# Performance work log

Hardware: AMD Instinct MI355X
Metric: run time of the kernel (lower is better)

The kernel has to match this reference:

```python
import jax, jax.numpy as jnp
import numpy as np

B, S, D, H, HD = 2, 2048, 1024, 16, 64
SCALE = HD ** -0.5


def setup_inputs() -> dict:
    key = jax.random.key(0)
    ks = jax.random.split(key, 11)
    w = 0.02
    return {
        "query": jax.random.normal(ks[0], (B, S, D), jnp.float32),
        "key": jax.random.normal(ks[1], (B, S, D), jnp.float32),
        "value": jax.random.normal(ks[2], (B, S, D), jnp.float32),
        "Wq": jax.random.normal(ks[3], (D, H * HD), jnp.float32) * w,
        "bq": jnp.zeros((H * HD,), jnp.float32),
        "Wk": jax.random.normal(ks[4], (D, H * HD), jnp.float32) * w,
        "bk": jnp.zeros((H * HD,), jnp.float32),
        "Wv": jax.random.normal(ks[5], (D, H * HD), jnp.float32) * w,
        "bv": jnp.zeros((H * HD,), jnp.float32),
        "Wo": jax.random.normal(ks[6], (H * HD, D), jnp.float32) * w,
        "bo": jnp.zeros((D,), jnp.float32),
    }


def reference(query, key, value, Wq, bq, Wk, bk, Wv, bv, Wo, bo):
    # projections -> [B, H, S, HD]
    q = (query @ Wq + bq).reshape(B, S, H, HD).transpose(0, 2, 1, 3)
    k = (key @ Wk + bk).reshape(B, S, H, HD).transpose(0, 2, 1, 3)
    v = (value @ Wv + bv).reshape(B, S, H, HD).transpose(0, 2, 1, 3)
    # attention scores [B, H, S, S]
    attn_score = jnp.einsum("bhqd,bhkd->bhqk", q, k) * SCALE
    attn_weights = jax.nn.softmax(attn_score, axis=-1)
    out = jnp.einsum("bhqk,bhkd->bhqd", attn_weights, v)
    out = out.transpose(0, 2, 1, 3).reshape(B, S, H * HD)
    out = out @ Wo + bo
    return out, attn_weights
```

## Files before the change

### kernel.cpp

```cpp
#include <hip/hip_runtime.h>
#include <hip/hip_bf16.h>
#include <stdint.h>

#define B_ 2
#define S_ 2048
#define D_ 1024
#define H_ 16
#define HD_ 64
#define SCALE_ 0.125f
#define SC2_ 0.18033688011112042f

typedef __attribute__((ext_vector_type(8))) short bfx8;
typedef __attribute__((ext_vector_type(4))) float f32x4;

#define VWAIT(n) asm volatile("s_waitcnt vmcnt(" #n ")" ::: "memory")

__device__ __forceinline__ void gld_lds16(const void* g, void* l) {
    __builtin_amdgcn_global_load_lds(
        (const __attribute__((address_space(1))) void*)g,
        (__attribute__((address_space(3))) void*)l, 16, 0, 0);
}

__global__ __launch_bounds__(256) void prep(
    const float* __restrict__ a, const float* __restrict__ b, const float* __restrict__ c,
    __hip_bfloat16* __restrict__ oa, __hip_bfloat16* __restrict__ ob, __hip_bfloat16* __restrict__ oc,
    const float* __restrict__ w0, const float* __restrict__ w1,
    const float* __restrict__ w2, const float* __restrict__ w3,
    __hip_bfloat16* __restrict__ o0, __hip_bfloat16* __restrict__ o1,
    __hip_bfloat16* __restrict__ o2, __hip_bfloat16* __restrict__ o3)
{
    __shared__ float t[32][33];
    const int bid = blockIdx.x;
    if (bid < 12288) {
        const int which = bid >> 12;
        const int xb = bid & 4095;
        const float* src = which == 0 ? a : which == 1 ? b : c;
        __hip_bfloat16* dst = which == 0 ? oa : which == 1 ? ob : oc;
        const size_t i = ((size_t)xb * 256 + threadIdx.x) * 4;
        float4 v = *(const float4*)(src + i);
        ushort4 u;
        __hip_bfloat16 tt;
        tt = __float2bfloat16(v.x); u.x = *(unsigned short*)&tt;
        tt = __float2bfloat16(v.y); u.y = *(unsigned short*)&tt;
        tt = __float2bfloat16(v.z); u.z = *(unsigned short*)&tt;
        tt = __float2bfloat16(v.w); u.w = *(unsigned short*)&tt;
        *(ushort4*)(dst + i) = u;
    } else {
        const int tb = bid - 12288;
        const int z = tb >> 10;
        const int rem = tb & 1023;
        const int bx = (rem & 31) * 32, by = (rem >> 5) * 32;
        const float* W = z == 0 ? w0 : z == 1 ? w1 : z == 2 ? w2 : w3;
        __hip_bfloat16* Wt = z == 0 ? o0 : z == 1 ? o1 : z == 2 ? o2 : o3;
        const int x = threadIdx.x & 31, y = threadIdx.x >> 5;
#pragma unroll
        for (int i = 0; i < 32; i += 8)
            t[y + i][x] = W[(size_t)(by + y + i) * 1024 + bx + x];
        __syncthreads();
#pragma unroll
        for (int i = 0; i < 32; i += 8)
            Wt[(size_t)(bx + y + i) * 1024 + by + x] = __float2bfloat16(t[x][y + i]);
    }
}

__global__ __launch_bounds__(256) void transpose_v(
    const __hip_bfloat16* __restrict__ vn,
    __hip_bfloat16* __restrict__ vtb)
{
    __shared__ unsigned int t[64][65];
    const int bh = blockIdx.y;
    const int st = blockIdx.x;
    const int tid = threadIdx.x, lane = tid & 63, w = tid >> 6;
    {
        const int sl = tid >> 2, c0 = (tid & 3) * 16;
        const ushort4* src = (const ushort4*)(vn + ((size_t)bh * S_ + st * 64 + sl) * 64 + c0);
        ushort4 a = src[0], b = src[1], c = src[2], d = src[3];
        unsigned short vals[16] = {a.x,a.y,a.z,a.w,b.x,b.y,b.z,b.w,
                                   c.x,c.y,c.z,c.w,d.x,d.y,d.z,d.w};
#pragma unroll
        for (int j = 0; j < 16; ++j) t[sl][c0 + j] = vals[j];
    }
    __syncthreads();
    const int sl2 = (lane & 31) * 2;
    const int dh  = (lane >> 5) * 8;
#pragma unroll
    for (int j = 0; j < 8; ++j) {
        const int d = w * 16 + dh + j;
        const unsigned int lo = t[sl2][d], hi = t[sl2 + 1][d];
        const unsigned int pk = (lo & 0xFFFFu) | (hi << 16);
        *(unsigned int*)(vtb + ((size_t)bh * HD_ + d) * S_ + st * 64 + sl2) = pk;
    }
}

__device__ __forceinline__ void gemm_body(
    const __hip_bfloat16* __restrict__ A,
    const __hip_bfloat16* __restrict__ Bt,
    const float* __restrict__ bias,
    void* __restrict__ Cout, int mode,
    __hip_bfloat16 (*As)[128 * 32], __hip_bfloat16 (*Bs)[128 * 32],
    int bm, int bn)
{
    constexpr int K = 1024, N = 1024;
    const int tid = threadIdx.x;
    const int wid = tid >> 6, lane = tid & 63;
    const int wm = (wid >> 1) * 64, wn = (wid & 1) * 64;

    f32x4 acc[4][4] = {};

    const int srow = lane >> 2;
    const int scol = (lane & 3) * 8;

    auto stage = [&](int kt, int buf) {
#pragma unroll
        for (int i = 0; i < 2; ++i) {
            const int rb = wid * 32 + i * 16;
            gld_lds16(A  + (size_t)(bm + rb + srow) * K + kt * 32 + scol, (char*)As[buf] + rb * 64);
            gld_lds16(Bt + (size_t)(bn + rb + srow) * K + kt * 32 + scol, (char*)Bs[buf] + rb * 64);
        }
    };

    stage(0, 0);
    __syncthreads();

    for (int kt = 0; kt < K / 32; ++kt) {
        const int cur = kt & 1;
        if (kt < K / 32 - 1) stage(kt + 1, cur ^ 1);
        bfx8 af[4], bf[4];
#pragma unroll
        for (int m = 0; m < 4; ++m)
            af[m] = *(const bfx8*)((const char*)As[cur] + (wm + m * 16 + (lane & 15)) * 64 + (lane >> 4) * 16);
#pragma unroll
        for (int n = 0; n < 4; ++n)
            bf[n] = *(const bfx8*)((const char*)Bs[cur] + (wn + n * 16 + (lane & 15)) * 64 + (lane >> 4) * 16);
        __builtin_amdgcn_s_setprio(1);
#pragma unroll
        for (int m = 0; m < 4; ++m)
#pragma unroll
            for (int n = 0; n < 4; ++n)
                acc[m][n] = __builtin_amdgcn_mfma_f32_16x16x32_bf16(af[m], bf[n], acc[m][n], 0, 0, 0);
        __builtin_amdgcn_s_setprio(0);
        __syncthreads();
    }

#pragma unroll
    for (int m = 0; m < 4; ++m) {
        const int row0 = bm + wm + m * 16 + ((lane >> 4) << 2);
#pragma unroll
        for (int n = 0; n < 4; ++n) {
            const int col = bn + wn + n * 16 + (lane & 15);
            const float bv = bias[col];
#pragma unroll
            for (int r = 0; r < 4; ++r) {
                const int i = row0 + r;
                const float v = acc[m][n][r] + bv;
                if (mode == 2) {
                    ((float*)Cout)[(size_t)i * N + col] = v;
                } else {
                    const int b = i >> 11, s = i & 2047, h = col >> 6, d = col & 63;
                    ((__hip_bfloat16*)Cout)[(((size_t)b * H_ + h) * S_ + s) * HD_ + d] = __float2bfloat16(v);
                }
            }
        }
    }
}

__global__ __launch_bounds__(256, 3) void gemm_qkv(
    const __hip_bfloat16* __restrict__ xq, const __hip_bfloat16* __restrict__ xk,
    const __hip_bfloat16* __restrict__ xv,
    const __hip_bfloat16* __restrict__ Wqt, const __hip_bfloat16* __restrict__ Wkt,
    const __hip_bfloat16* __restrict__ Wvt,
    const float* __restrict__ bq, const float* __restrict__ bk, const float* __restrict__ bv,
    __hip_bfloat16* __restrict__ qb, __hip_bfloat16* __restrict__ kbuf,
    __hip_bfloat16* __restrict__ vnb)
{
    __shared__ __align__(16) __hip_bfloat16 As[2][128 * 32];
    __shared__ __align__(16) __hip_bfloat16 Bs[2][128 * 32];
    const int z = blockIdx.z;
    const __hip_bfloat16* A  = z == 0 ? xq : z == 1 ? xk : xv;
    const __hip_bfloat16* Bt = z == 0 ? Wqt : z == 1 ? Wkt : Wvt;
    const float* bias        = z == 0 ? bq : z == 1 ? bk : bv;
    void* out                = z == 0 ? (void*)qb : z == 1 ? (void*)kbuf : (void*)vnb;
    gemm_body(A, Bt, bias, out, 0, As, Bs, blockIdx.x * 128, blockIdx.y * 128);
}

__global__ __launch_bounds__(256, 2) void gemm_wo(
    const __hip_bfloat16* __restrict__ A, const __hip_bfloat16* __restrict__ Bt,
    const float* __restrict__ bias, float* __restrict__ Cout)
{
    constexpr int K = 1024, N = 1024;
    __shared__ __align__(16) __hip_bfloat16 As[2][128 * 32];
    __shared__ __align__(16) __hip_bfloat16 Bs[2][64 * 32];
    const int tid = threadIdx.x;
    const int wid = tid >> 6, lane = tid & 63;
    const int wm = (wid >> 1) * 64, wn = (wid & 1) * 32;
    const int bm = blockIdx.x * 128, bn = blockIdx.y * 64;

    f32x4 acc[4][2] = {};

    const int srow = lane >> 2;
    const int scol = (lane & 3) * 8;

    auto stage = [&](int kt, int buf) {
#pragma unroll
        for (int i = 0; i < 2; ++i) {
            const int rb = wid * 32 + i * 16;
            gld_lds16(A + (size_t)(bm + rb + srow) * K + kt * 32 + scol, (char*)As[buf] + rb * 64);
        }
        const int rbB = wid * 16;
        gld_lds16(Bt + (size_t)(bn + rbB + srow) * K + kt * 32 + scol, (char*)Bs[buf] + rbB * 64);
    };

    stage(0, 0);
    __syncthreads();

    for (int kt = 0; kt < K / 32; ++kt) {
        const int cur = kt & 1;
        if (kt < K / 32 - 1) stage(kt + 1, cur ^ 1);
        bfx8 af[4], bf[2];
#pragma unroll
        for (int m = 0; m < 4; ++m)
            af[m] = *(const bfx8*)((const char*)As[cur] + (wm + m * 16 + (lane & 15)) * 64 + (lane >> 4) * 16);
#pragma unroll
        for (int n = 0; n < 2; ++n)
            bf[n] = *(const bfx8*)((const char*)Bs[cur] + (wn + n * 16 + (lane & 15)) * 64 + (lane >> 4) * 16);
        __builtin_amdgcn_s_setprio(1);
#pragma unroll
        for (int m = 0; m < 4; ++m)
#pragma unroll
            for (int n = 0; n < 2; ++n)
                acc[m][n] = __builtin_amdgcn_mfma_f32_16x16x32_bf16(af[m], bf[n], acc[m][n], 0, 0, 0);
        __builtin_amdgcn_s_setprio(0);
        __syncthreads();
    }

#pragma unroll
    for (int m = 0; m < 4; ++m) {
        const int row0 = bm + wm + m * 16 + ((lane >> 4) << 2);
#pragma unroll
        for (int n = 0; n < 2; ++n) {
            const int col = bn + wn + n * 16 + (lane & 15);
            const float bv = bias[col];
#pragma unroll
            for (int r = 0; r < 4; ++r)
                Cout[(size_t)(row0 + r) * N + col] = acc[m][n][r] + bv;
        }
    }
}

__global__ __launch_bounds__(256, 4) void attn_fused(
    const __hip_bfloat16* __restrict__ qb,
    const __hip_bfloat16* __restrict__ kb,
    const __hip_bfloat16* __restrict__ vt,
    float* __restrict__ attnw,
    __hip_bfloat16* __restrict__ aout)
{
    __shared__ __align__(16) char lds_[40960];
    char* const ps_ = lds_ + 32768;

    const int wg  = blockIdx.x;
    const int lin = (wg & 7) * 128 + (wg >> 3);
    const int bh  = lin >> 5;
    const int qt  = lin & 31;

    const int tid = threadIdx.x, wid = tid >> 6, lane = tid & 63;
    const int qrow0 = qt * 64 + wid * 16;

    const char* kh = (const char*)(kb + (size_t)bh * S_ * HD_);
    const char* vh = (const char*)(vt + (size_t)bh * HD_ * S_);

    bfx8 qf[2];
#pragma unroll
    for (int kx = 0; kx < 2; ++kx)
        qf[kx] = *(const bfx8*)(qb + ((size_t)bh * S_ + qrow0 + (lane & 15)) * HD_
                                 + kx * 32 + (lane >> 4) * 8);

    const int sr = lane >> 3;
    const int sc = lane & 7;

    auto stage_k = [&](int kt, char* dst) {
#pragma unroll
        for (int i = 0; i < 2; ++i) {
            const int rb = wid * 16 + i * 8;
            const int row = rb + sr;
            const int colb = (sc * 16) ^ ((row & 7) << 4);
            gld_lds16(kh + (size_t)(kt * 64 + row) * 128 + colb, dst + rb * 128);
        }
    };
    auto stage_v = [&](int kt, char* dst) {
#pragma unroll
        for (int i = 0; i < 2; ++i) {
            const int rb = wid * 16 + i * 8;
            const int row = rb + sr;
            const int colb = (sc * 16) ^ ((row & 7) << 4);
            gld_lds16(vh + ((size_t)row * S_ + kt * 64) * 2 + colb, dst + rb * 128);
        }
    };

    float lsum = 0.f;
    stage_k(0, lds_);
    stage_k(1, lds_ + 8192);
    for (int kt = 0; kt < 32; ++kt) {
        if (kt < 30) {
            stage_k(kt + 2, lds_ + ((kt + 2) & 3) * 8192);
            VWAIT(4);
        } else if (kt == 30) { VWAIT(2); } else { VWAIT(0); }
        __builtin_amdgcn_sched_barrier(0);
        __builtin_amdgcn_s_barrier();

        const char* kbase = lds_ + (kt & 3) * 8192;
        f32x4 c[4] = {};
#pragma unroll
        for (int kx = 0; kx < 2; ++kx) {
            bfx8 bfv[4];
#pragma unroll
            for (int cf = 0; cf < 4; ++cf) {
                const int row = cf * 16 + (lane & 15);
                bfv[cf] = *(const bfx8*)(kbase + row * 128
                                          + ((kx * 64 + (lane >> 4) * 16) ^ ((row & 7) << 4)));
            }
            __builtin_amdgcn_s_setprio(1);
#pragma unroll
            for (int cf = 0; cf < 4; ++cf)
                c[cf] = __builtin_amdgcn_mfma_f32_16x16x32_bf16(bfv[cf], qf[kx], c[cf], 0, 0, 0);
            __builtin_amdgcn_s_setprio(0);
        }
#pragma unroll
        for (int cf = 0; cf < 4; ++cf)
            lsum += exp2f(c[cf][0] * SC2_) + exp2f(c[cf][1] * SC2_)
                  + exp2f(c[cf][2] * SC2_) + exp2f(c[cf][3] * SC2_);
    }
    float llog;
    {
        float s = lsum;
        s += __shfl_xor(s, 16);
        s += __shfl_xor(s, 32);
        llog = -__log2f(s);
    }

    f32x4 o[4] = {};
    stage_k(0, lds_);
    stage_v(0, lds_ + 16384);
    VWAIT(0);
    __builtin_amdgcn_s_barrier();
    for (int kt = 0; kt < 32; ++kt) {
        const int cur = kt & 1;
        const char* ksb = lds_ + cur * 8192;
        const char* vsb = lds_ + 16384 + cur * 8192;

        if (kt < 31) {
            stage_k(kt + 1, lds_ + (cur ^ 1) * 8192);
            stage_v(kt + 1, lds_ + 16384 + (cur ^ 1) * 8192);
        }

        f32x4 c[4] = {};
#pragma unroll
        for (int kx = 0; kx < 2; ++kx) {
            bfx8 bfv[4];
#pragma unroll
            for (int cf = 0; cf < 4; ++cf) {
                const int row = cf * 16 + (lane & 15);
                bfv[cf] = *(const bfx8*)(ksb + row * 128
                                          + ((kx * 64 + (lane >> 4) * 16) ^ ((row & 7) << 4)));
            }
            __builtin_amdgcn_s_setprio(1);
#pragma unroll
            for (int cf = 0; cf < 4; ++cf)
                c[cf] = __builtin_amdgcn_mfma_f32_16x16x32_bf16(bfv[cf], qf[kx], c[cf], 0, 0, 0);
            __builtin_amdgcn_s_setprio(0);
        }

        {
            const int q = lane & 15;
            char* const prow_base = ps_ + (wid * 16 + q) * 128;
            const int swz = (q & 7) << 4;
#pragma unroll
            for (int cf = 0; cf < 4; ++cf) {
                const int k0b = (cf * 16 + (lane >> 4) * 4) * 2;
                ushort4 pk;
                __hip_bfloat16 bb;
                bb = __float2bfloat16(exp2f(fmaf(c[cf][0], SC2_, llog))); pk.x = *(unsigned short*)&bb;
                bb = __float2bfloat16(exp2f(fmaf(c[cf][1], SC2_, llog))); pk.y = *(unsigned short*)&bb;
                bb = __float2bfloat16(exp2f(fmaf(c[cf][2], SC2_, llog))); pk.z = *(unsigned short*)&bb;
                bb = __float2bfloat16(exp2f(fmaf(c[cf][3], SC2_, llog))); pk.w = *(unsigned short*)&bb;
                *(ushort4*)(prow_base + (k0b ^ swz)) = pk;
            }
        }

#pragma unroll
        for (int rr = 0; rr < 4; ++rr) {
            const int p = wid * 16 + rr * 4 + (lane >> 4);
            const uint2 u = *(const uint2*)(ps_ + p * 128
                                            + (((lane & 15) * 8) ^ ((p & 7) << 4)));
            f32x4 f;
            f[0] = __uint_as_float(u.x << 16);
            f[1] = __uint_as_float(u.x & 0xFFFF0000u);
            f[2] = __uint_as_float(u.y << 16);
            f[3] = __uint_as_float(u.y & 0xFFFF0000u);
            __builtin_nontemporal_store(f,
                (f32x4*)(attnw + ((size_t)bh * S_ + qt * 64 + p) * S_ + kt * 64 + (lane & 15) * 4));
        }

#pragma unroll
        for (int kx = 0; kx < 2; ++kx) {
            bfx8 pf, vf[4];
            {
                const int prow = wid * 16 + (lane & 15);
                pf = *(const bfx8*)(ps_ + prow * 128
                                     + ((kx * 64 + (lane >> 4) * 16) ^ ((prow & 7) << 4)));
            }
#pragma unroll
            for (int df = 0; df < 4; ++df) {
                const int vrow = df * 16 + (lane & 15);
                vf[df] = *(const bfx8*)(vsb + vrow * 128
                                         + ((kx * 64 + (lane >> 4) * 16) ^ ((vrow & 7) << 4)));
            }
            __builtin_amdgcn_s_setprio(1);
#pragma unroll
            for (int df = 0; df < 4; ++df)
                o[df] = __builtin_amdgcn_mfma_f32_16x16x32_bf16(pf, vf[df], o[df], 0, 0, 0);
            __builtin_amdgcn_s_setprio(0);
        }

        if (kt < 31) {
            VWAIT(4);
            __builtin_amdgcn_sched_barrier(0);
            __builtin_amdgcn_s_barrier();
        }
    }

    const int b = bh >> 4, h = bh & 15;
#pragma unroll
    for (int r = 0; r < 4; ++r) {
        const int s = qrow0 + ((lane >> 4) << 2) + r;
#pragma unroll
        for (int df = 0; df < 4; ++df) {
            const int d = df * 16 + (lane & 15);
            aout[((size_t)b * S_ + s) * D_ + h * HD_ + d] = __float2bfloat16(o[df][r]);
        }
    }
}

extern "C" void kernel_launch(void* const* d_in, const int* in_sizes, int n_in,
                              void* d_out, int out_size, void* d_ws, size_t ws_size,
                              hipStream_t stream)
{
    (void)in_sizes; (void)n_in; (void)out_size; (void)ws_size;
    const float* query = (const float*)d_in[0];
    const float* key_  = (const float*)d_in[1];
    const float* value = (const float*)d_in[2];
    const float* Wq = (const float*)d_in[3];
    const float* bq = (const float*)d_in[4];
    const float* Wk = (const float*)d_in[5];
    const float* bk = (const float*)d_in[6];
    const float* Wv = (const float*)d_in[7];
    const float* bv = (const float*)d_in[8];
    const float* Wo = (const float*)d_in[9];
    const float* bo = (const float*)d_in[10];

    char* ws = (char*)d_ws;
    const size_t MB = 1u << 20;
    __hip_bfloat16* xq   = (__hip_bfloat16*)(ws + 0 * MB);
    __hip_bfloat16* xk   = (__hip_bfloat16*)(ws + 8 * MB);
    __hip_bfloat16* xv   = (__hip_bfloat16*)(ws + 16 * MB);
    __hip_bfloat16* Wqt  = (__hip_bfloat16*)(ws + 24 * MB);
    __hip_bfloat16* Wkt  = (__hip_bfloat16*)(ws + 26 * MB);
    __hip_bfloat16* Wvt  = (__hip_bfloat16*)(ws + 28 * MB);
    __hip_bfloat16* Wot  = (__hip_bfloat16*)(ws + 30 * MB);
    __hip_bfloat16* qb   = (__hip_bfloat16*)(ws + 32 * MB);
    __hip_bfloat16* kbuf = (__hip_bfloat16*)(ws + 40 * MB);
    __hip_bfloat16* vtb  = (__hip_bfloat16*)(ws + 48 * MB);
    __hip_bfloat16* vnb  = (__hip_bfloat16*)(ws + 56 * MB);
    __hip_bfloat16* aout = (__hip_bfloat16*)(ws + 56 * MB);

    float* outp  = (float*)d_out;
    float* attnw = outp + (size_t)B_ * S_ * D_;

    prep<<<dim3(16384), 256, 0, stream>>>(query, key_, value, xq, xk, xv,
                                          Wq, Wk, Wv, Wo, Wqt, Wkt, Wvt, Wot);
    gemm_qkv<<<dim3(32, 8, 3), 256, 0, stream>>>(xq, xk, xv, Wqt, Wkt, Wvt, bq, bk, bv, qb, kbuf, vnb);
    transpose_v<<<dim3(32, 32), 256, 0, stream>>>(vnb, vtb);
    attn_fused<<<dim3(1024), 256, 0, stream>>>(qb, kbuf, vtb, attnw, aout);
    gemm_wo<<<dim3(32, 16), 256, 0, stream>>>(aout, Wot, bo, outp);
}
```

Measured before the change: 201.2 us.

## Process two query tiles per workgroup to share K staging in softmax-sum pass

Each attention workgroup now handles two 64-row query tiles of the same head, halving the grid to 512 blocks. The first pass, which accumulates softmax denominators, loads each K tile into LDS once and runs MFMAs for both query tiles, halving K traffic for that pass. The second pass still runs separately per tile, so K/V are staged twice there. In exchange the kernel needs more registers, and with 512 blocks on 256 CUs occupancy and latency hiding may drop.

```diff
diff --git a/kernel.cpp b/kernel.cpp
--- a/kernel.cpp
+++ b/kernel.cpp
@@ -258,21 +258,24 @@
     char* const ps_ = lds_ + 32768;
 
     const int wg  = blockIdx.x;
-    const int lin = (wg & 7) * 128 + (wg >> 3);
-    const int bh  = lin >> 5;
-    const int qt  = lin & 31;
+    const int lin = (wg & 7) * 64 + (wg >> 3);
+    const int bh  = lin >> 4;
+    const int jj  = lin & 15;
+    const int qtA = jj * 2, qtB = jj * 2 + 1;
 
     const int tid = threadIdx.x, wid = tid >> 6, lane = tid & 63;
-    const int qrow0 = qt * 64 + wid * 16;
 
     const char* kh = (const char*)(kb + (size_t)bh * S_ * HD_);
     const char* vh = (const char*)(vt + (size_t)bh * HD_ * S_);
 
-    bfx8 qf[2];
-#pragma unroll
-    for (int kx = 0; kx < 2; ++kx)
-        qf[kx] = *(const bfx8*)(qb + ((size_t)bh * S_ + qrow0 + (lane & 15)) * HD_
-                                 + kx * 32 + (lane >> 4) * 8);
+    bfx8 qfA[2], qfB[2];
+#pragma unroll
+    for (int kx = 0; kx < 2; ++kx) {
+        qfA[kx] = *(const bfx8*)(qb + ((size_t)bh * S_ + qtA * 64 + wid * 16 + (lane & 15)) * HD_
+                                  + kx * 32 + (lane >> 4) * 8);
+        qfB[kx] = *(const bfx8*)(qb + ((size_t)bh * S_ + qtB * 64 + wid * 16 + (lane & 15)) * HD_
+                                  + kx * 32 + (lane >> 4) * 8);
+    }
 
     const int sr = lane >> 3;
     const int sc = lane & 7;
@@ -296,7 +299,7 @@
         }
     };
 
-    float lsum = 0.f;
+    float lsumA = 0.f, lsumB = 0.f;
     stage_k(0, lds_);
     stage_k(1, lds_ + 8192);
     for (int kt = 0; kt < 32; ++kt) {
@@ -308,7 +311,7 @@
         __builtin_amdgcn_s_barrier();
 
         const char* kbase = lds_ + (kt & 3) * 8192;
-        f32x4 c[4] = {};
+        f32x4 cA[4] = {}, cB[4] = {};
 #pragma unroll
         for (int kx = 0; kx < 2; ++kx) {
             bfx8 bfv[4];
@@ -321,122 +324,141 @@
             __builtin_amdgcn_s_setprio(1);
 #pragma unroll
             for (int cf = 0; cf < 4; ++cf)
-                c[cf] = __builtin_amdgcn_mfma_f32_16x16x32_bf16(bfv[cf], qf[kx], c[cf], 0, 0, 0);
+                cA[cf] = __builtin_amdgcn_mfma_f32_16x16x32_bf16(bfv[cf], qfA[kx], cA[cf], 0, 0, 0);
+#pragma unroll
+            for (int cf = 0; cf < 4; ++cf)
+                cB[cf] = __builtin_amdgcn_mfma_f32_16x16x32_bf16(bfv[cf], qfB[kx], cB[cf], 0, 0, 0);
             __builtin_amdgcn_s_setprio(0);
         }
 #pragma unroll
-        for (int cf = 0; cf < 4; ++cf)
-            lsum += exp2f(c[cf][0] * SC2_) + exp2f(c[cf][1] * SC2_)
-                  + exp2f(c[cf][2] * SC2_) + exp2f(c[cf][3] * SC2_);
-    }
-    float llog;
+        for (int cf = 0; cf < 4; ++cf) {
+            lsumA += exp2f(cA[cf][0] * SC2_) + exp2f(cA[cf][1] * SC2_)
+                   + exp2f(cA[cf][2] * SC2_) + exp2f(cA[cf][3] * SC2_);
+            lsumB += exp2f(cB[cf][0] * SC2_) + exp2f(cB[cf][1] * SC2_)
+                   + exp2f(cB[cf][2] * SC2_) + exp2f(cB[cf][3] * SC2_);
+        }
+    }
+    float llogA, llogB;
     {
-        float s = lsum;
-        s += __shfl_xor(s, 16);
-        s += __shfl_xor(s, 32);
-        llog = -__log2f(s);
-    }
-
-    f32x4 o[4] = {};
-    stage_k(0, lds_);
-    stage_v(0, lds_ + 16384);
-    VWAIT(0);
-    __builtin_amdgcn_s_barrier();
-    for (int kt = 0; kt < 32; ++kt) {
-        const int cur = kt & 1;
-        const char* ksb = lds_ + cur * 8192;
-        const char* vsb = lds_ + 16384 + cur * 8192;
-
-        if (kt < 31) {
-            stage_k(kt + 1, lds_ + (cur ^ 1) * 8192);
-            stage_v(kt + 1, lds_ + 16384 + (cur ^ 1) * 8192);
-        }
-
-        f32x4 c[4] = {};
-#pragma unroll
-        for (int kx = 0; kx < 2; ++kx) {
-            bfx8 bfv[4];
-#pragma unroll
-            for (int cf = 0; cf < 4; ++cf) {
-                const int row = cf * 16 + (lane & 15);
-                bfv[cf] = *(const bfx8*)(ksb + row * 128
-                                          + ((kx * 64 + (lane >> 4) * 16) ^ ((row & 7) << 4)));
-            }
-            __builtin_amdgcn_s_setprio(1);
-#pragma unroll
-            for (int cf = 0; cf < 4; ++cf)
-                c[cf] = __builtin_amdgcn_mfma_f32_16x16x32_bf16(bfv[cf], qf[kx], c[cf], 0, 0, 0);
-            __builtin_amdgcn_s_setprio(0);
-        }
-
-        {
-            const int q = lane & 15;
-            char* const prow_base = ps_ + (wid * 16 + q) * 128;
-            const int swz = (q & 7) << 4;
-#pragma unroll
-            for (int cf = 0; cf < 4; ++cf) {
-                const int k0b = (cf * 16 + (lane >> 4) * 4) * 2;
-                ushort4 pk;
-                __hip_bfloat16 bb;
-                bb = __float2bfloat16(exp2f(fmaf(c[cf][0], SC2_, llog))); pk.x = *(unsigned short*)&bb;
-                bb = __float2bfloat16(exp2f(fmaf(c[cf][1], SC2_, llog))); pk.y = *(unsigned short*)&bb;
-                bb = __float2bfloat16(exp2f(fmaf(c[cf][2], SC2_, llog))); pk.z = *(unsigned short*)&bb;
-                bb = __float2bfloat16(exp2f(fmaf(c[cf][3], SC2_, llog))); pk.w = *(unsigned short*)&bb;
-                *(ushort4*)(prow_base + (k0b ^ swz)) = pk;
-            }
-        }
-
-#pragma unroll
-        for (int rr = 0; rr < 4; ++rr) {
-            const int p = wid * 16 + rr * 4 + (lane >> 4);
-            const uint2 u = *(const uint2*)(ps_ + p * 128
-                                            + (((lane & 15) * 8) ^ ((p & 7) << 4)));
-            f32x4 f;
-            f[0] = __uint_as_float(u.x << 16);
-            f[1] = __uint_as_float(u.x & 0xFFFF0000u);
-            f[2] = __uint_as_float(u.y << 16);
-            f[3] = __uint_as_float(u.y & 0xFFFF0000u);
-            __builtin_nontemporal_store(f,
-                (f32x4*)(attnw + ((size_t)bh * S_ + qt * 64 + p) * S_ + kt * 64 + (lane & 15) * 4));
-        }
-
-#pragma unroll
-        for (int kx = 0; kx < 2; ++kx) {
-            bfx8 pf, vf[4];
+        float s = lsumA;
+        s += __shfl_xor(s, 16); s += __shfl_xor(s, 32);
+        llogA = -__log2f(s);
+        float u = lsumB;
+        u += __shfl_xor(u, 16); u += __shfl_xor(u, 32);
+        llogB = -__log2f(u);
+    }
+
+#pragma unroll
+    for (int half = 0; half < 2; ++half) {
+        const int qt = half == 0 ? qtA : qtB;
+        const float llog = half == 0 ? llogA : llogB;
+        const bfx8 qh0 = half == 0 ? qfA[0] : qfB[0];
+        const bfx8 qh1 = half == 0 ? qfA[1] : qfB[1];
+        const int qrow0 = qt * 64 + wid * 16;
+
+        f32x4 o[4] = {};
+        stage_k(0, lds_);
+        stage_v(0, lds_ + 16384);
+        VWAIT(0);
+        __builtin_amdgcn_s_barrier();
+        for (int kt = 0; kt < 32; ++kt) {
+            const int cur = kt & 1;
+            const char* ksb = lds_ + cur * 8192;
+            const char* vsb = lds_ + 16384 + cur * 8192;
+
+            if (kt < 31) {
+                stage_k(kt + 1, lds_ + (cur ^ 1) * 8192);
+                stage_v(kt + 1, lds_ + 16384 + (cur ^ 1) * 8192);
+            }
+
+            f32x4 c[4] = {};
+#pragma unroll
+            for (int kx = 0; kx < 2; ++kx) {
+                const bfx8 qf = kx == 0 ? qh0 : qh1;
+                bfx8 bfv[4];
+#pragma unroll
+                for (int cf = 0; cf < 4; ++cf) {
+                    const int row = cf * 16 + (lane & 15);
+                    bfv[cf] = *(const bfx8*)(ksb + row * 128
+                                              + ((kx * 64 + (lane >> 4) * 16) ^ ((row & 7) << 4)));
+                }
+                __builtin_amdgcn_s_setprio(1);
+#pragma unroll
+                for (int cf = 0; cf < 4; ++cf)
+                    c[cf] = __builtin_amdgcn_mfma_f32_16x16x32_bf16(bfv[cf], qf, c[cf], 0, 0, 0);
+                __builtin_amdgcn_s_setprio(0);
+            }
+
             {
-                const int prow = wid * 16 + (lane & 15);
-                pf = *(const bfx8*)(ps_ + prow * 128
-                                     + ((kx * 64 + (lane >> 4) * 16) ^ ((prow & 7) << 4)));
-            }
+                const int q = lane & 15;
+                char* const prow_base = ps_ + (wid * 16 + q) * 128;
+                const int swz = (q & 7) << 4;
+#pragma unroll
+                for (int cf = 0; cf < 4; ++cf) {
+                    const int k0b = (cf * 16 + (lane >> 4) * 4) * 2;
+                    ushort4 pk;
+                    __hip_bfloat16 bb;
+                    bb = __float2bfloat16(exp2f(fmaf(c[cf][0], SC2_, llog))); pk.x = *(unsigned short*)&bb;
+                    bb = __float2bfloat16(exp2f(fmaf(c[cf][1], SC2_, llog))); pk.y = *(unsigned short*)&bb;
+                    bb = __float2bfloat16(exp2f(fmaf(c[cf][2], SC2_, llog))); pk.z = *(unsigned short*)&bb;
+                    bb = __float2bfloat16(exp2f(fmaf(c[cf][3], SC2_, llog))); pk.w = *(unsigned short*)&bb;
+                    *(ushort4*)(prow_base + (k0b ^ swz)) = pk;
+                }
+            }
+
+#pragma unroll
+            for (int rr = 0; rr < 4; ++rr) {
+                const int p = wid * 16 + rr * 4 + (lane >> 4);
+                const uint2 u = *(const uint2*)(ps_ + p * 128
+                                                + (((lane & 15) * 8) ^ ((p & 7) << 4)));
+                f32x4 f;
+                f[0] = __uint_as_float(u.x << 16);
+                f[1] = __uint_as_float(u.x & 0xFFFF0000u);
+                f[2] = __uint_as_float(u.y << 16);
+                f[3] = __uint_as_float(u.y & 0xFFFF0000u);
+                __builtin_nontemporal_store(f,
+                    (f32x4*)(attnw + ((size_t)bh * S_ + qt * 64 + p) * S_ + kt * 64 + (lane & 15) * 4));
+            }
+
+#pragma unroll
+            for (int kx = 0; kx < 2; ++kx) {
+                bfx8 pf, vf[4];
+                {
+                    const int prow = wid * 16 + (lane & 15);
+                    pf = *(const bfx8*)(ps_ + prow * 128
+                                         + ((kx * 64 + (lane >> 4) * 16) ^ ((prow & 7) << 4)));
+                }
+#pragma unroll
+                for (int df = 0; df < 4; ++df) {
+                    const int vrow = df * 16 + (lane & 15);
+                    vf[df] = *(const bfx8*)(vsb + vrow * 128
+                                             + ((kx * 64 + (lane >> 4) * 16) ^ ((vrow & 7) << 4)));
+                }
+                __builtin_amdgcn_s_setprio(1);
+#pragma unroll
+                for (int df = 0; df < 4; ++df)
+                    o[df] = __builtin_amdgcn_mfma_f32_16x16x32_bf16(pf, vf[df], o[df], 0, 0, 0);
+                __builtin_amdgcn_s_setprio(0);
+            }
+
+            if (kt < 31) {
+                VWAIT(4);
+                __builtin_amdgcn_sched_barrier(0);
+                __builtin_amdgcn_s_barrier();
+            }
+        }
+
+        const int b = bh >> 4, h = bh & 15;
+#pragma unroll
+        for (int r = 0; r < 4; ++r) {
+            const int s = qrow0 + ((lane >> 4) << 2) + r;
 #pragma unroll
             for (int df = 0; df < 4; ++df) {
-                const int vrow = df * 16 + (lane & 15);
-                vf[df] = *(const bfx8*)(vsb + vrow * 128
-                                         + ((kx * 64 + (lane >> 4) * 16) ^ ((vrow & 7) << 4)));
-            }
-            __builtin_amdgcn_s_setprio(1);
-#pragma unroll
-            for (int df = 0; df < 4; ++df)
-                o[df] = __builtin_amdgcn_mfma_f32_16x16x32_bf16(pf, vf[df], o[df], 0, 0, 0);
-            __builtin_amdgcn_s_setprio(0);
-        }
-
-        if (kt < 31) {
-            VWAIT(4);
-            __builtin_amdgcn_sched_barrier(0);
-            __builtin_amdgcn_s_barrier();
-        }
-    }
-
-    const int b = bh >> 4, h = bh & 15;
-#pragma unroll
-    for (int r = 0; r < 4; ++r) {
-        const int s = qrow0 + ((lane >> 4) << 2) + r;
-#pragma unroll
-        for (int df = 0; df < 4; ++df) {
-            const int d = df * 16 + (lane & 15);
-            aout[((size_t)b * S_ + s) * D_ + h * HD_ + d] = __float2bfloat16(o[df][r]);
-        }
+                const int d = df * 16 + (lane & 15);
+                aout[((size_t)b * S_ + s) * D_ + h * HD_ + d] = __float2bfloat16(o[df][r]);
+            }
+        }
+
     }
 }
 
@@ -479,6 +501,6 @@
                                           Wq, Wk, Wv, Wo, Wqt, Wkt, Wvt, Wot);
     gemm_qkv<<<dim3(32, 8, 3), 256, 0, stream>>>(xq, xk, xv, Wqt, Wkt, Wvt, bq, bk, bv, qb, kbuf, vnb);
     transpose_v<<<dim3(32, 32), 256, 0, stream>>>(vnb, vtb);
-    attn_fused<<<dim3(1024), 256, 0, stream>>>(qb, kbuf, vtb, attnw, aout);
+    attn_fused<<<dim3(512), 256, 0, stream>>>(qb, kbuf, vtb, attnw, aout);
     gemm_wo<<<dim3(32, 16), 256, 0, stream>>>(aout, Wot, bo, outp);
 }
```

New measurement: 225.1 us. 11.9% more time.
